# Performance work log

Measured on AMD Instinct MI355X. Metric: run time of the kernel, lower is better.

The kernel has to match this reference:

```python
import jax, jax.numpy as jnp
import numpy as np

INPUT_DIM = 2048
NUM_EXPERTS = 64
TOP_K = 2


def setup_inputs() -> dict:
    key = jax.random.key(0)
    kx, kw, kb = jax.random.split(key, 3)
    x = jax.random.normal(kx, (4, 4096, INPUT_DIM), dtype=jnp.float32)
    # nn.Linear default init: U(-1/sqrt(fan_in), 1/sqrt(fan_in))
    bound = 1.0 / np.sqrt(INPUT_DIM)
    W = jax.random.uniform(kw, (INPUT_DIM, NUM_EXPERTS), dtype=jnp.float32, minval=-bound, maxval=bound)
    b = jax.random.uniform(kb, (NUM_EXPERTS,), dtype=jnp.float32, minval=-bound, maxval=bound)
    return {"x": x, "W": W, "b": b}


def reference(x, W, b):
    # dropout p=0.0 -> identity
    logits = jnp.einsum("bsd,de->bse", x, W) + b            # [B,S,E]
    topk_logits, topk_idx = jax.lax.top_k(logits, TOP_K)     # [B,S,K]
    topk_w = jax.nn.softmax(topk_logits, axis=-1)            # softmax over top-k only
    # scatter top-k weights back to full expert dim; non-top-k stay zero
    onehot = jax.nn.one_hot(topk_idx, NUM_EXPERTS, dtype=topk_w.dtype)  # [B,S,K,E]
    weights = jnp.einsum("bsk,bske->bse", topk_w, onehot)
    return weights
```

## Files before the change

### kernel.cpp

```cpp
#include <hip/hip_runtime.h>
#include <math.h>

#define D 2048
#define E 64
#define TOK 64

typedef float4 f4;

__device__ __forceinline__ float fget(const float4 v, int j) {
    return j == 0 ? v.x : j == 1 ? v.y : j == 2 ? v.z : v.w;
}

__device__ __forceinline__ void fmablock(float (&acc)[8][8],
                                         const float4 (&xw)[2],
                                         const float4 (&ww)[2]) {
#pragma unroll
    for (int t = 0; t < 8; ++t) {
        const float xt = fget(t < 4 ? xw[0] : xw[1], t & 3);
#pragma unroll
        for (int e = 0; e < 8; ++e) {
            const float we = fget(e < 4 ? ww[0] : ww[1], e & 3);
            acc[t][e] = fmaf(xt, we, acc[t][e]);
        }
    }
}

__device__ __forceinline__ void tile_store(float* b, const float (&acc)[8][8],
                                           int tg, int eg) {
#pragma unroll
    for (int t = 0; t < 8; ++t) {
        f4 v0 = {acc[t][0], acc[t][1], acc[t][2], acc[t][3]};
        f4 v1 = {acc[t][4], acc[t][5], acc[t][6], acc[t][7]};
        *(f4*)(b + (tg * 8 + t) * 64 + eg * 8) = v0;
        *(f4*)(b + (tg * 8 + t) * 64 + eg * 8 + 4) = v1;
    }
}

__device__ __forceinline__ void tile_addin(const float* b, float (&acc)[8][8],
                                           int tg, int eg) {
#pragma unroll
    for (int t = 0; t < 8; ++t) {
        f4 v0 = *(const f4*)(b + (tg * 8 + t) * 64 + eg * 8);
        f4 v1 = *(const f4*)(b + (tg * 8 + t) * 64 + eg * 8 + 4);
        acc[t][0] += v0.x; acc[t][1] += v0.y; acc[t][2] += v0.z; acc[t][3] += v0.w;
        acc[t][4] += v1.x; acc[t][5] += v1.y; acc[t][6] += v1.z; acc[t][7] += v1.w;
    }
}

#define NQ 8
#define KQ (D / NQ)
#define KCH (KQ / 2)
#define SK 16
#define NSTEP (KCH / SK)

__global__ __launch_bounds__(128)
void gating_mm(const float* __restrict__ x, const float* __restrict__ W,
               float* __restrict__ partial, int ntok)
{
    __shared__ __align__(16) float smem[8192];

    const int tid  = threadIdx.x;
    const int lane = tid & 63;
    const int w    = __builtin_amdgcn_readfirstlane(tid >> 6);
    const int tg   = lane >> 3;
    const int eg   = lane & 7;
    const int q    = blockIdx.x & 7;
    const int tok0 = (blockIdx.x >> 3) * TOK;

    float* base  = smem + w * 4096;
    float* xbuf0 = base;
    float* xbuf1 = base + 1024;
    float* wbuf0 = base + 2048;
    float* wbuf1 = base + 3072;

    const float* xg = x + (size_t)(tok0 + lane) * D + q * KQ + w * KCH;
    const float* wg = W + (size_t)(q * KQ + w * KCH) * E;

    float acc[8][8];
#pragma unroll
    for (int t = 0; t < 8; ++t)
#pragma unroll
        for (int e = 0; e < 8; ++e) acc[t][e] = 0.f;

    float4 xs[4];
    float  ws[16];
#pragma unroll
    for (int c = 0; c < 4; ++c) xs[c] = *(const f4*)(xg + c * 4);
#pragma unroll
    for (int j = 0; j < 16; ++j) ws[j] = wg[j * E + lane];
#pragma unroll
    for (int j = 0; j < 16; ++j) xbuf0[j * 64 + lane] = fget(xs[j >> 2], j & 3);
#pragma unroll
    for (int j = 0; j < 16; ++j) wbuf0[j * 64 + lane] = ws[j];
#pragma unroll
    for (int c = 0; c < 4; ++c) xs[c] = *(const f4*)(xg + SK + c * 4);
#pragma unroll
    for (int j = 0; j < 16; ++j) ws[j] = wg[(SK + j) * E + lane];

    float4 xw[2][2], ww[2][2];
    xw[0][0] = *(const f4*)(xbuf0 + tg * 8);
    xw[0][1] = *(const f4*)(xbuf0 + tg * 8 + 4);
    ww[0][0] = *(const f4*)(wbuf0 + eg * 8);
    ww[0][1] = *(const f4*)(wbuf0 + eg * 8 + 4);
    xw[1][0] = *(const f4*)(xbuf0 + 64 + tg * 8);
    xw[1][1] = *(const f4*)(xbuf0 + 64 + tg * 8 + 4);
    ww[1][0] = *(const f4*)(wbuf0 + 64 + eg * 8);
    ww[1][1] = *(const f4*)(wbuf0 + 64 + eg * 8 + 4);

#pragma unroll 1
    for (int s = 0; s < NSTEP; ++s) {
        float* xc = (s & 1) ? xbuf1 : xbuf0;
        float* wc = (s & 1) ? wbuf1 : wbuf0;
        float* xn = (s & 1) ? xbuf0 : xbuf1;
        float* wn = (s & 1) ? wbuf0 : wbuf1;
        if (s < NSTEP - 1) {
#pragma unroll
            for (int j = 0; j < 16; ++j) xn[j * 64 + lane] = fget(xs[j >> 2], j & 3);
#pragma unroll
            for (int j = 0; j < 16; ++j) wn[j * 64 + lane] = ws[j];
            const int s2 = (s + 2 < NSTEP) ? s + 2 : NSTEP - 1;
#pragma unroll
            for (int c = 0; c < 4; ++c) xs[c] = *(const f4*)(xg + s2 * SK + c * 4);
#pragma unroll
            for (int j = 0; j < 16; ++j) ws[j] = wg[(s2 * SK + j) * E + lane];
        }
        const float* xnx = (s < NSTEP - 1) ? xn : xc;
        const float* wnx = (s < NSTEP - 1) ? wn : wc;
#pragma unroll
        for (int r = 0; r < SK; ++r) {
            const int p = r & 1;
            fmablock(acc, xw[p], ww[p]);
            const float* xsrc = (r < SK - 2) ? (xc + (r + 2) * 64)
                                             : (xnx + (r - (SK - 2)) * 64);
            const float* wsrc = (r < SK - 2) ? (wc + (r + 2) * 64)
                                             : (wnx + (r - (SK - 2)) * 64);
            xw[p][0] = *(const f4*)(xsrc + tg * 8);
            xw[p][1] = *(const f4*)(xsrc + tg * 8 + 4);
            ww[p][0] = *(const f4*)(wsrc + eg * 8);
            ww[p][1] = *(const f4*)(wsrc + eg * 8 + 4);
        }
    }

    __syncthreads();
    if (w == 1) tile_store(smem, acc, tg, eg);
    __syncthreads();
    if (w == 0) {
        tile_addin(smem, acc, tg, eg);
        float* pq = partial + ((size_t)q * ntok + tok0) * E;
#pragma unroll
        for (int t = 0; t < 8; ++t) {
            f4 v0 = {acc[t][0], acc[t][1], acc[t][2], acc[t][3]};
            f4 v1 = {acc[t][4], acc[t][5], acc[t][6], acc[t][7]};
            *(f4*)(pq + (tg * 8 + t) * E + eg * 8) = v0;
            *(f4*)(pq + (tg * 8 + t) * E + eg * 8 + 4) = v1;
        }
    }
}

__global__ __launch_bounds__(256)
void gating_topk(const float* __restrict__ partial, const float* __restrict__ Bv,
                 float* __restrict__ out, int ntok)
{
    __shared__ float logits[64][65];
    __shared__ float sw1[64], sw2[64];
    __shared__ int   si1[64], si2[64];

    const int tid  = threadIdx.x;
    const int tok0 = blockIdx.x * 64;
    const int tok  = tid >> 2;
    const int seg  = tid & 3;
    {
        float4 s[4];
        const float* p0 = partial + ((size_t)tok0 + tok) * E + seg * 16;
#pragma unroll
        for (int c = 0; c < 4; ++c) s[c] = *(const f4*)(p0 + 4 * c);
#pragma unroll
        for (int q = 1; q < NQ; ++q) {
            const float* p = partial + ((size_t)q * ntok + tok0 + tok) * E + seg * 16;
#pragma unroll
            for (int c = 0; c < 4; ++c) {
                f4 v = *(const f4*)(p + 4 * c);
                s[c].x += v.x; s[c].y += v.y; s[c].z += v.z; s[c].w += v.w;
            }
        }
#pragma unroll
        for (int c = 0; c < 4; ++c) {
            f4 bv = *(const f4*)(Bv + seg * 16 + 4 * c);
            logits[tok][seg * 16 + 4*c + 0] = s[c].x + bv.x;
            logits[tok][seg * 16 + 4*c + 1] = s[c].y + bv.y;
            logits[tok][seg * 16 + 4*c + 2] = s[c].z + bv.z;
            logits[tok][seg * 16 + 4*c + 3] = s[c].w + bv.w;
        }
    }
    __syncthreads();

    if (tid < 64) {
        float m1 = -3.4e38f, m2 = -3.4e38f;
        int i1 = 0, i2 = 0;
#pragma unroll
        for (int e = 0; e < E; ++e) {
            float v = logits[tid][e];
            if (v > m1)      { m2 = m1; i2 = i1; m1 = v; i1 = e; }
            else if (v > m2) { m2 = v; i2 = e; }
        }
        float p = 1.0f / (1.0f + expf(m2 - m1));
        sw1[tid] = p; sw2[tid] = 1.0f - p;
        si1[tid] = i1; si2[tid] = i2;
    }
    __syncthreads();

    float4* o4 = (float4*)(out + (size_t)tok0 * E);
#pragma unroll
    for (int p5 = 0; p5 < 4; ++p5) {
        int idx = tid + p5 * 256;
        int tl  = idx >> 4;
        int e0  = (idx & 15) * 4;
        int a1 = si1[tl], a2 = si2[tl];
        float v1 = sw1[tl], v2 = sw2[tl];
        float4 v;
        v.x = (e0 + 0 == a1) ? v1 : (e0 + 0 == a2) ? v2 : 0.0f;
        v.y = (e0 + 1 == a1) ? v1 : (e0 + 1 == a2) ? v2 : 0.0f;
        v.z = (e0 + 2 == a1) ? v1 : (e0 + 2 == a2) ? v2 : 0.0f;
        v.w = (e0 + 3 == a1) ? v1 : (e0 + 3 == a2) ? v2 : 0.0f;
        o4[idx] = v;
    }
}

#define FKCH 512
#define FSK 16
#define FNSTEP (FKCH / FSK)

__device__ __forceinline__ void fb_tile_store(float* b, const float (&acc)[8][8],
                                              int tg, int eg) {
#pragma unroll
    for (int t = 0; t < 8; ++t) {
        f4 v0 = {acc[t][0], acc[t][1], acc[t][2], acc[t][3]};
        f4 v1 = {acc[t][4], acc[t][5], acc[t][6], acc[t][7]};
        *(f4*)(b + (tg * 8 + t) * 65 + eg * 8) = v0;
        *(f4*)(b + (tg * 8 + t) * 65 + eg * 8 + 4) = v1;
    }
}

__device__ __forceinline__ void fb_tile_addin(const float* b, float (&acc)[8][8],
                                              int tg, int eg) {
#pragma unroll
    for (int t = 0; t < 8; ++t) {
        f4 v0 = *(const f4*)(b + (tg * 8 + t) * 65 + eg * 8);
        f4 v1 = *(const f4*)(b + (tg * 8 + t) * 65 + eg * 8 + 4);
        acc[t][0] += v0.x; acc[t][1] += v0.y; acc[t][2] += v0.z; acc[t][3] += v0.w;
        acc[t][4] += v1.x; acc[t][5] += v1.y; acc[t][6] += v1.z; acc[t][7] += v1.w;
    }
}

__global__ __launch_bounds__(256)
void gating_fb(const float* __restrict__ x, const float* __restrict__ W,
               const float* __restrict__ Bv, float* __restrict__ out)
{
    __shared__ __align__(16) float smem[16384];

    const int tid  = threadIdx.x;
    const int lane = tid & 63;
    const int w    = __builtin_amdgcn_readfirstlane(tid >> 6);
    const int tg   = lane >> 3;
    const int eg   = lane & 7;
    const int tok0 = blockIdx.x * TOK;

    float* base  = smem + w * 4096;
    float* xbuf0 = base;
    float* xbuf1 = base + 1024;
    float* wbuf0 = base + 2048;
    float* wbuf1 = base + 3072;

    const float* xg = x + (size_t)(tok0 + lane) * D + w * FKCH;
    const float* wg = W + (size_t)w * FKCH * E;

    float acc[8][8];
#pragma unroll
    for (int t = 0; t < 8; ++t)
#pragma unroll
        for (int e = 0; e < 8; ++e) acc[t][e] = 0.f;

    float4 xs[4];
    float  ws[16];
#pragma unroll
    for (int c = 0; c < 4; ++c) xs[c] = *(const f4*)(xg + c * 4);
#pragma unroll
    for (int j = 0; j < 16; ++j) ws[j] = wg[j * E + lane];
#pragma unroll
    for (int j = 0; j < 16; ++j) xbuf0[j * 64 + lane] = fget(xs[j >> 2], j & 3);
#pragma unroll
    for (int j = 0; j < 16; ++j) wbuf0[j * 64 + lane] = ws[j];
#pragma unroll
    for (int c = 0; c < 4; ++c) xs[c] = *(const f4*)(xg + FSK + c * 4);
#pragma unroll
    for (int j = 0; j < 16; ++j) ws[j] = wg[(FSK + j) * E + lane];

    float4 xw[2][2], ww[2][2];
    xw[0][0] = *(const f4*)(xbuf0 + tg * 8);
    xw[0][1] = *(const f4*)(xbuf0 + tg * 8 + 4);
    ww[0][0] = *(const f4*)(wbuf0 + eg * 8);
    ww[0][1] = *(const f4*)(wbuf0 + eg * 8 + 4);
    xw[1][0] = *(const f4*)(xbuf0 + 64 + tg * 8);
    xw[1][1] = *(const f4*)(xbuf0 + 64 + tg * 8 + 4);
    ww[1][0] = *(const f4*)(wbuf0 + 64 + eg * 8);
    ww[1][1] = *(const f4*)(wbuf0 + 64 + eg * 8 + 4);

#pragma unroll 1
    for (int s = 0; s < FNSTEP; ++s) {
        float* xc = (s & 1) ? xbuf1 : xbuf0;
        float* wc = (s & 1) ? wbuf1 : wbuf0;
        float* xn = (s & 1) ? xbuf0 : xbuf1;
        float* wn = (s & 1) ? wbuf0 : wbuf1;
        if (s < FNSTEP - 1) {
#pragma unroll
            for (int j = 0; j < 16; ++j) xn[j * 64 + lane] = fget(xs[j >> 2], j & 3);
#pragma unroll
            for (int j = 0; j < 16; ++j) wn[j * 64 + lane] = ws[j];
            const int s2 = (s + 2 < FNSTEP) ? s + 2 : FNSTEP - 1;
#pragma unroll
            for (int c = 0; c < 4; ++c) xs[c] = *(const f4*)(xg + s2 * FSK + c * 4);
#pragma unroll
            for (int j = 0; j < 16; ++j) ws[j] = wg[(s2 * FSK + j) * E + lane];
        }
        const float* xnx = (s < FNSTEP - 1) ? xn : xc;
        const float* wnx = (s < FNSTEP - 1) ? wn : wc;
#pragma unroll
        for (int r = 0; r < FSK; ++r) {
            const int p = r & 1;
            fmablock(acc, xw[p], ww[p]);
            const float* xsrc = (r < FSK - 2) ? (xc + (r + 2) * 64)
                                              : (xnx + (r - (FSK - 2)) * 64);
            const float* wsrc = (r < FSK - 2) ? (wc + (r + 2) * 64)
                                              : (wnx + (r - (FSK - 2)) * 64);
            xw[p][0] = *(const f4*)(xsrc + tg * 8);
            xw[p][1] = *(const f4*)(xsrc + tg * 8 + 4);
            ww[p][0] = *(const f4*)(wsrc + eg * 8);
            ww[p][1] = *(const f4*)(wsrc + eg * 8 + 4);
        }
    }

    float* buf0 = smem;
    float* buf1 = smem + 4160;
    __syncthreads();
    if (w == 2) fb_tile_store(buf0, acc, tg, eg);
    if (w == 3) fb_tile_store(buf1, acc, tg, eg);
    __syncthreads();
    if (w == 0) fb_tile_addin(buf0, acc, tg, eg);
    if (w == 1) fb_tile_addin(buf1, acc, tg, eg);
    __syncthreads();
    if (w == 1) fb_tile_store(buf0, acc, tg, eg);
    __syncthreads();
    if (w == 0) {
        fb_tile_addin(buf0, acc, tg, eg);
        fb_tile_store(buf0, acc, tg, eg);
    }
    __syncthreads();

    float* logits = buf0;
    float* sw1 = smem + 8320; float* sw2 = smem + 8384;
    int*   si1 = (int*)(smem + 8448); int* si2 = (int*)(smem + 8512);

    if (w == 0) {
        float m1 = -3.4e38f, m2 = -3.4e38f;
        int i1 = 0, i2 = 0;
#pragma unroll
        for (int e = 0; e < E; ++e) {
            float v = logits[lane * 65 + e] + Bv[e];
            if (v > m1)      { m2 = m1; i2 = i1; m1 = v; i1 = e; }
            else if (v > m2) { m2 = v; i2 = e; }
        }
        float p = 1.0f / (1.0f + expf(m2 - m1));
        sw1[lane] = p; sw2[lane] = 1.0f - p;
        si1[lane] = i1; si2[lane] = i2;
    }
    __syncthreads();

    float4* o4 = (float4*)(out + (size_t)tok0 * E);
#pragma unroll
    for (int p5 = 0; p5 < 4; ++p5) {
        int idx = tid + p5 * 256;
        int tl  = idx >> 4;
        int e0  = (idx & 15) * 4;
        int a1 = si1[tl], a2 = si2[tl];
        float v1 = sw1[tl], v2 = sw2[tl];
        float4 v;
        v.x = (e0 + 0 == a1) ? v1 : (e0 + 0 == a2) ? v2 : 0.0f;
        v.y = (e0 + 1 == a1) ? v1 : (e0 + 1 == a2) ? v2 : 0.0f;
        v.z = (e0 + 2 == a1) ? v1 : (e0 + 2 == a2) ? v2 : 0.0f;
        v.w = (e0 + 3 == a1) ? v1 : (e0 + 3 == a2) ? v2 : 0.0f;
        o4[idx] = v;
    }
}

extern "C" void kernel_launch(void* const* d_in, const int* in_sizes, int n_in,
                              void* d_out, int out_size, void* d_ws, size_t ws_size,
                              hipStream_t stream) {
    const float* x = (const float*)d_in[0];
    const float* W = (const float*)d_in[1];
    const float* b = (const float*)d_in[2];
    float* out = (float*)d_out;

    const int tokens = in_sizes[0] / D;
    const size_t need = (size_t)NQ * tokens * E * sizeof(float);

    if (d_ws != nullptr && ws_size >= need && (tokens % TOK) == 0) {
        gating_mm<<<(tokens / TOK) * NQ, 128, 0, stream>>>(x, W, (float*)d_ws, tokens);
        gating_topk<<<tokens / TOK, 256, 0, stream>>>((const float*)d_ws, b, out, tokens);
    } else {
        gating_fb<<<tokens / TOK, 256, 0, stream>>>(x, W, b, out);
    }
}
```

Measured before the change: 229.6 us.

## Single-buffer LDS staging interleaved with FMA rows in gating matmul

Replaces the double-buffered shared-memory staging with one buffer per wave. Each staging write is placed just after the row it overwrites has been read into registers, so global-to-LDS copies are spread across the FMA loop instead of batched at the start of each step. W is now loaded as float4 instead of 16 scalar loads, and the step loop is manually unrolled with template flags to drop runtime branches. This halves LDS use and is meant to raise occupancy and overlap, but it relies on a tight in-wave ordering of reads and writes with no barrier, which is fragile.

Result: slower. 251.9 us (+9.7%).

```diff
diff --git a/kernel.cpp b/kernel.cpp
--- a/kernel.cpp
+++ b/kernel.cpp
@@ -53,11 +53,54 @@
 #define SK 16
 #define NSTEP (KCH / SK)
 
+template<bool STAGE, bool LOAD>
+__device__ __forceinline__ void step_body(
+    float (&acc)[8][8], float4 (&xw)[2][2], float4 (&ww)[2][2],
+    float* xbuf, float* wbuf, int tg, int eg, int lane, int wso,
+    float4 (&xsC)[4], float4 (&xsN)[4], float4 (&ws)[4],
+    const float* xg, const float* wgl, int s2)
+{
+#pragma unroll
+    for (int r = 0; r < 16; ++r) {
+        const int p = r & 1;
+        fmablock(acc, xw[p], ww[p]);
+        if (STAGE) {
+            xbuf[r * 64 + lane] = fget(xsC[r >> 2], r & 3);
+            if (r == 6) {
+                *(f4*)(wbuf + wso) = ws[0];
+                *(f4*)(wbuf + wso + 32) = ws[1];
+            }
+            if (r == 14) {
+                *(f4*)(wbuf + 512 + wso) = ws[2];
+                *(f4*)(wbuf + 512 + wso + 32) = ws[3];
+            }
+        }
+        if (LOAD) {
+            if (r == 0) {
+#pragma unroll
+                for (int c = 0; c < 4; ++c)
+                    xsN[c] = *(const f4*)(xg + s2 * SK + c * 4);
+            }
+            if (r == 15) {
+                ws[0] = *(const f4*)(wgl + (size_t)s2 * SK * E);
+                ws[1] = *(const f4*)(wgl + (size_t)s2 * SK * E + 32);
+                ws[2] = *(const f4*)(wgl + (size_t)(s2 * SK + 8) * E);
+                ws[3] = *(const f4*)(wgl + (size_t)(s2 * SK + 8) * E + 32);
+            }
+        }
+        const int pr = (r + 2) & 15;
+        xw[p][0] = *(const f4*)(xbuf + pr * 64 + tg * 8);
+        xw[p][1] = *(const f4*)(xbuf + pr * 64 + tg * 8 + 4);
+        ww[p][0] = *(const f4*)(wbuf + pr * 64 + eg * 8);
+        ww[p][1] = *(const f4*)(wbuf + pr * 64 + eg * 8 + 4);
+    }
+}
+
 __global__ __launch_bounds__(128)
 void gating_mm(const float* __restrict__ x, const float* __restrict__ W,
                float* __restrict__ partial, int ntok)
 {
-    __shared__ __align__(16) float smem[8192];
+    __shared__ __align__(16) float smem[4096];
 
     const int tid  = threadIdx.x;
     const int lane = tid & 63;
@@ -67,14 +110,13 @@
     const int q    = blockIdx.x & 7;
     const int tok0 = (blockIdx.x >> 3) * TOK;
 
-    float* base  = smem + w * 4096;
-    float* xbuf0 = base;
-    float* xbuf1 = base + 1024;
-    float* wbuf0 = base + 2048;
-    float* wbuf1 = base + 3072;
-
-    const float* xg = x + (size_t)(tok0 + lane) * D + q * KQ + w * KCH;
-    const float* wg = W + (size_t)(q * KQ + w * KCH) * E;
+    float* xbuf = smem + w * 2048;
+    float* wbuf = xbuf + 1024;
+
+    const float* xg  = x + (size_t)(tok0 + lane) * D + q * KQ + w * KCH;
+    const float* wg  = W + (size_t)(q * KQ + w * KCH) * E;
+    const float* wgl = wg + (size_t)(lane >> 3) * E + (lane & 7) * 4;
+    const int    wso = (lane >> 3) * 64 + (lane & 7) * 4;
 
     float acc[8][8];
 #pragma unroll
@@ -82,64 +124,47 @@
 #pragma unroll
         for (int e = 0; e < 8; ++e) acc[t][e] = 0.f;
 
-    float4 xs[4];
-    float  ws[16];
-#pragma unroll
-    for (int c = 0; c < 4; ++c) xs[c] = *(const f4*)(xg + c * 4);
-#pragma unroll
-    for (int j = 0; j < 16; ++j) ws[j] = wg[j * E + lane];
-#pragma unroll
-    for (int j = 0; j < 16; ++j) xbuf0[j * 64 + lane] = fget(xs[j >> 2], j & 3);
-#pragma unroll
-    for (int j = 0; j < 16; ++j) wbuf0[j * 64 + lane] = ws[j];
-#pragma unroll
-    for (int c = 0; c < 4; ++c) xs[c] = *(const f4*)(xg + SK + c * 4);
-#pragma unroll
-    for (int j = 0; j < 16; ++j) ws[j] = wg[(SK + j) * E + lane];
+    float4 xsA[4], xsB[4], ws[4];
+#pragma unroll
+    for (int c = 0; c < 4; ++c) xsA[c] = *(const f4*)(xg + c * 4);
+    ws[0] = *(const f4*)(wgl);
+    ws[1] = *(const f4*)(wgl + 32);
+    ws[2] = *(const f4*)(wgl + 8 * E);
+    ws[3] = *(const f4*)(wgl + 8 * E + 32);
+#pragma unroll
+    for (int j = 0; j < 16; ++j) xbuf[j * 64 + lane] = fget(xsA[j >> 2], j & 3);
+    *(f4*)(wbuf + wso) = ws[0];
+    *(f4*)(wbuf + wso + 32) = ws[1];
+    *(f4*)(wbuf + 512 + wso) = ws[2];
+    *(f4*)(wbuf + 512 + wso + 32) = ws[3];
+#pragma unroll
+    for (int c = 0; c < 4; ++c) xsA[c] = *(const f4*)(xg + SK + c * 4);
+    ws[0] = *(const f4*)(wgl + (size_t)SK * E);
+    ws[1] = *(const f4*)(wgl + (size_t)SK * E + 32);
+    ws[2] = *(const f4*)(wgl + (size_t)(SK + 8) * E);
+    ws[3] = *(const f4*)(wgl + (size_t)(SK + 8) * E + 32);
 
     float4 xw[2][2], ww[2][2];
-    xw[0][0] = *(const f4*)(xbuf0 + tg * 8);
-    xw[0][1] = *(const f4*)(xbuf0 + tg * 8 + 4);
-    ww[0][0] = *(const f4*)(wbuf0 + eg * 8);
-    ww[0][1] = *(const f4*)(wbuf0 + eg * 8 + 4);
-    xw[1][0] = *(const f4*)(xbuf0 + 64 + tg * 8);
-    xw[1][1] = *(const f4*)(xbuf0 + 64 + tg * 8 + 4);
-    ww[1][0] = *(const f4*)(wbuf0 + 64 + eg * 8);
-    ww[1][1] = *(const f4*)(wbuf0 + 64 + eg * 8 + 4);
+    xw[0][0] = *(const f4*)(xbuf + tg * 8);
+    xw[0][1] = *(const f4*)(xbuf + tg * 8 + 4);
+    ww[0][0] = *(const f4*)(wbuf + eg * 8);
+    ww[0][1] = *(const f4*)(wbuf + eg * 8 + 4);
+    xw[1][0] = *(const f4*)(xbuf + 64 + tg * 8);
+    xw[1][1] = *(const f4*)(xbuf + 64 + tg * 8 + 4);
+    ww[1][0] = *(const f4*)(wbuf + 64 + eg * 8);
+    ww[1][1] = *(const f4*)(wbuf + 64 + eg * 8 + 4);
 
 #pragma unroll 1
-    for (int s = 0; s < NSTEP; ++s) {
-        float* xc = (s & 1) ? xbuf1 : xbuf0;
-        float* wc = (s & 1) ? wbuf1 : wbuf0;
-        float* xn = (s & 1) ? xbuf0 : xbuf1;
-        float* wn = (s & 1) ? wbuf0 : wbuf1;
-        if (s < NSTEP - 1) {
-#pragma unroll
-            for (int j = 0; j < 16; ++j) xn[j * 64 + lane] = fget(xs[j >> 2], j & 3);
-#pragma unroll
-            for (int j = 0; j < 16; ++j) wn[j * 64 + lane] = ws[j];
-            const int s2 = (s + 2 < NSTEP) ? s + 2 : NSTEP - 1;
-#pragma unroll
-            for (int c = 0; c < 4; ++c) xs[c] = *(const f4*)(xg + s2 * SK + c * 4);
-#pragma unroll
-            for (int j = 0; j < 16; ++j) ws[j] = wg[(s2 * SK + j) * E + lane];
-        }
-        const float* xnx = (s < NSTEP - 1) ? xn : xc;
-        const float* wnx = (s < NSTEP - 1) ? wn : wc;
-#pragma unroll
-        for (int r = 0; r < SK; ++r) {
-            const int p = r & 1;
-            fmablock(acc, xw[p], ww[p]);
-            const float* xsrc = (r < SK - 2) ? (xc + (r + 2) * 64)
-                                             : (xnx + (r - (SK - 2)) * 64);
-            const float* wsrc = (r < SK - 2) ? (wc + (r + 2) * 64)
-                                             : (wnx + (r - (SK - 2)) * 64);
-            xw[p][0] = *(const f4*)(xsrc + tg * 8);
-            xw[p][1] = *(const f4*)(xsrc + tg * 8 + 4);
-            ww[p][0] = *(const f4*)(wsrc + eg * 8);
-            ww[p][1] = *(const f4*)(wsrc + eg * 8 + 4);
-        }
-    }
+    for (int ss = 0; ss < 3; ++ss) {
+        step_body<true, true>(acc, xw, ww, xbuf, wbuf, tg, eg, lane, wso,
+                              xsA, xsB, ws, xg, wgl, 2 * ss + 2);
+        step_body<true, true>(acc, xw, ww, xbuf, wbuf, tg, eg, lane, wso,
+                              xsB, xsA, ws, xg, wgl, 2 * ss + 3);
+    }
+    step_body<true, false>(acc, xw, ww, xbuf, wbuf, tg, eg, lane, wso,
+                           xsA, xsB, ws, xg, wgl, 0);
+    step_body<false, false>(acc, xw, ww, xbuf, wbuf, tg, eg, lane, wso,
+                            xsB, xsA, ws, xg, wgl, 0);
 
     __syncthreads();
     if (w == 1) tile_store(smem, acc, tg, eg);
```
